# Kernel optimization log

Hardware: AMD Instinct MI355X
Metric: run time of the kernel (lower is better)

## Reference

```python
import jax, jax.numpy as jnp
import numpy as np

N = 50000      # nodes
E = 400000     # edges
IN = 128       # in_dim == emb_dim (residual requires equality)
POS = 64       # pos_in_dim
EMB = 128
LN_EPS = 1e-5


def _ln(x, g, b):
    m = jnp.mean(x, axis=-1, keepdims=True)
    v = jnp.mean((x - m) ** 2, axis=-1, keepdims=True)
    return (x - m) / jnp.sqrt(v + LN_EPS) * g + b


def _gin(x, src, dst, eps, W1, b1, g1, be1, W2, b2):
    # GINConv: mlp((1+eps)*x + sum_{j in N(i)} x_j)
    agg = jax.ops.segment_sum(x[src], dst, num_segments=x.shape[0])
    h = (1.0 + eps) * x + agg
    h = jax.nn.relu(_ln(h @ W1 + b1, g1, be1))
    return h @ W2 + b2


def setup_inputs() -> dict:
    key = jax.random.key(0)
    ks = jax.random.split(key, 8)
    x = jax.random.normal(ks[0], (N, IN), jnp.float32)
    pos = jax.random.normal(ks[1], (N, POS), jnp.float32)
    edge_index = jax.random.randint(ks[2], (2, E), 0, N)
    d = IN + POS
    f32 = jnp.float32
    W1 = (jax.random.normal(ks[3], (d, EMB), f32) / np.sqrt(d))
    W2 = (jax.random.normal(ks[4], (EMB, EMB), f32) / np.sqrt(EMB))
    W1p = (jax.random.normal(ks[5], (POS, EMB), f32) / np.sqrt(POS))
    W2p = (jax.random.normal(ks[6], (EMB, EMB), f32) / np.sqrt(EMB))
    z = jnp.zeros((EMB,), f32)
    o = jnp.ones((EMB,), f32)
    return {
        "x": x, "pos": pos, "edge_index": edge_index,
        "eps": jnp.zeros((), f32), "W1": W1, "b1": z, "g1": o, "be1": z,
        "W2": W2, "b2": z, "ln_g": o, "ln_b": z,
        "epsp": jnp.zeros((), f32), "W1p": W1p, "b1p": z, "g1p": o, "be1p": z,
        "W2p": W2p, "b2p": z, "lnp_g": o, "lnp_b": z,
    }


def reference(x, pos, edge_index, eps, W1, b1, g1, be1, W2, b2, ln_g, ln_b,
              epsp, W1p, b1p, g1p, be1p, W2p, b2p, lnp_g, lnp_b):
    src, dst = edge_index[0], edge_index[1]
    node_feats = jnp.concatenate([x, pos], axis=-1)  # [N, IN+POS]
    h = jax.nn.relu(_ln(_gin(node_feats, src, dst, eps, W1, b1, g1, be1, W2, b2), ln_g, ln_b))
    p = jax.nn.relu(_ln(_gin(pos, src, dst, epsp, W1p, b1p, g1p, be1p, W2p, b2p), lnp_g, lnp_b))
    # dropout is identity in eval mode (model_drop_ratio applied only when training)
    h = h + x  # add_residual=True
    return (h, p)
```

## Files before the change

### kernel.cpp

```cpp
#include <hip/hip_runtime.h>

#define NN    50000
#define NPAD  50048
#define HB    391
#define EE    400000
#define IND   128
#define POSD  64
#define DD    192
#define EMBD  128
#define LNEPS 1e-5f
#define CAP   32

#define FILLV_B 391
#define CAT_B   4692
#define WC_B    256

typedef __attribute__((ext_vector_type(8))) short bf16x8;
typedef __attribute__((ext_vector_type(4))) unsigned short u16x4;
typedef __attribute__((ext_vector_type(4))) float f32x4;
typedef unsigned short ushort_t;
typedef unsigned int uint_t;

#define MFMA16 __builtin_amdgcn_mfma_f32_16x16x32_bf16

__device__ inline ushort_t f2bf(float f) {
  union { float f; unsigned u; } v; v.f = f;
  unsigned r = (v.u + 0x7FFFu + ((v.u >> 16) & 1u)) >> 16;
  return (ushort_t)r;
}
__device__ inline float bf2f(unsigned u) {
  union { unsigned u; float f; } v; v.u = u << 16;
  return v.f;
}

__global__ __launch_bounds__(256) void prep_k(
    const float* __restrict__ x, const float* __restrict__ pos,
    const int* __restrict__ ei,
    const float* __restrict__ W1, const float* __restrict__ W2,
    const float* __restrict__ W1p, const float* __restrict__ W2p,
    int* __restrict__ cnt, int* __restrict__ csr,
    ushort_t* __restrict__ cat, ushort_t* __restrict__ wt) {
  const int bid = blockIdx.x;
  if (bid < FILLV_B) {
    int e0 = (bid * 256 + threadIdx.x) * 4;
    if (e0 >= EE) return;
    int4 s = *(const int4*)(ei + e0);
    int4 d = *(const int4*)(ei + EE + e0);
    int i0 = atomicAdd(&cnt[d.x], 1);
    int i1 = atomicAdd(&cnt[d.y], 1);
    int i2 = atomicAdd(&cnt[d.z], 1);
    int i3 = atomicAdd(&cnt[d.w], 1);
    if (i0 < CAP) csr[(size_t)d.x * CAP + i0] = s.x;
    if (i1 < CAP) csr[(size_t)d.y * CAP + i1] = s.y;
    if (i2 < CAP) csr[(size_t)d.z * CAP + i2] = s.z;
    if (i3 < CAP) csr[(size_t)d.w * CAP + i3] = s.w;
  } else if (bid < FILLV_B + CAT_B) {
    int id  = (bid - FILLV_B) * 256 + threadIdx.x;
    int n   = id / 24, sub = id - n * 24;
    bf16x8 o = (bf16x8){0, 0, 0, 0, 0, 0, 0, 0};
    if (n < NN) {
      const float* src = (sub < 16) ? (x + (size_t)n * IND + sub * 8)
                                    : (pos + (size_t)n * POSD + (sub - 16) * 8);
      f32x4 v0 = *(const f32x4*)(src);
      f32x4 v1 = *(const f32x4*)(src + 4);
#pragma unroll
      for (int i = 0; i < 4; ++i) {
        o[i]     = (short)f2bf(v0[i]);
        o[i + 4] = (short)f2bf(v1[i]);
      }
    }
    *(bf16x8*)(cat + (size_t)n * DD + sub * 8) = o;
  } else {
    int t = (bid - FILLV_B - CAT_B) * 256 + threadIdx.x;
    if (t < 24576) {
      int c = t / 192, k = t % 192;
      wt[t] = f2bf(W1[k * EMBD + c]);
    } else if (t < 40960) {
      int q = t - 24576; int c = q / 128, k = q % 128;
      wt[t] = f2bf(W2[k * EMBD + c]);
    } else if (t < 49152) {
      int q = t - 40960; int c = q / 64, k = q % 64;
      wt[t] = f2bf(W1p[k * EMBD + c]);
    } else {
      int q = t - 49152; int c = q / 128, k = q % 128;
      wt[t] = f2bf(W2p[k * EMBD + c]);
    }
  }
}

__global__ __launch_bounds__(256) void gather2_k(
    const ushort_t* __restrict__ cat, const int* __restrict__ cnt,
    const int* __restrict__ csr,
    const float* __restrict__ epsv, const float* __restrict__ epspv,
    ushort_t* __restrict__ h0, ushort_t* __restrict__ p0) {
  const int lane = threadIdx.x & 63;
  const int wv   = threadIdx.x >> 6;
  const int half = lane >> 5;
  const int l2   = lane & 31;
  const int n    = blockIdx.x * 8 + wv * 2 + half;

  int deg = 0;
  if (n < NN) { deg = cnt[n]; if (deg > CAP) deg = CAP; }
  int idx = (l2 < deg) ? csr[(size_t)n * CAP + l2] : NN;

  float a0 = 0.f, a1 = 0.f, a2 = 0.f, a3 = 0.f, a4 = 0.f, a5 = 0.f;
  for (int t = 0; t < deg; t += 8) {
    int s[8];
#pragma unroll
    for (int k = 0; k < 8; ++k) s[k] = __shfl(idx, half * 32 + t + k);
    u16x4 u[8]; uint_t v[8];
#pragma unroll
    for (int k = 0; k < 8; ++k) {
      int sk = (t + k < CAP) ? s[k] : NN;
      const ushort_t* r = cat + (size_t)sk * DD;
      u[k] = *(const u16x4*)(r + l2 * 4);
      v[k] = *(const uint_t*)(r + 128 + l2 * 2);
    }
#pragma unroll
    for (int k = 0; k < 8; ++k) {
      a0 += bf2f(u[k][0]); a1 += bf2f(u[k][1]);
      a2 += bf2f(u[k][2]); a3 += bf2f(u[k][3]);
      a4 += bf2f(v[k] & 0xffffu); a5 += bf2f(v[k] >> 16);
    }
  }

  const float e1  = 1.0f + epsv[0];
  const float ep1 = 1.0f + epspv[0];
  const ushort_t* self = cat + (size_t)n * DD;
  u16x4 su = *(const u16x4*)(self + l2 * 4);
  uint_t sv = *(const uint_t*)(self + 128 + l2 * 2);

  u16x4 o;
  o[0] = f2bf(fmaf(e1, bf2f(su[0]), a0));
  o[1] = f2bf(fmaf(e1, bf2f(su[1]), a1));
  o[2] = f2bf(fmaf(e1, bf2f(su[2]), a2));
  o[3] = f2bf(fmaf(e1, bf2f(su[3]), a3));
  *(u16x4*)(h0 + (size_t)n * DD + l2 * 4) = o;

  float p4 = bf2f(sv & 0xffffu), p5 = bf2f(sv >> 16);
  uint_t oh = (uint_t)f2bf(fmaf(e1, p4, a4)) |
              ((uint_t)f2bf(fmaf(e1, p5, a5)) << 16);
  *(uint_t*)(h0 + (size_t)n * DD + 128 + l2 * 2) = oh;
  uint_t op = (uint_t)f2bf(fmaf(ep1, p4, a4)) |
              ((uint_t)f2bf(fmaf(ep1, p5, a5)) << 16);
  *(uint_t*)(p0 + (size_t)n * POSD + l2 * 2) = op;
}

__device__ inline void ln_epi_T(f32x4 (&acc)[8][2],
                                const float* __restrict__ bias,
                                const float* __restrict__ gam,
                                const float* __restrict__ bet, int g) {
  f32x4 bv[8], gv[8], bev[8];
#pragma unroll
  for (int nt = 0; nt < 8; ++nt) {
    bv[nt]  = *(const f32x4*)(bias + nt * 16 + g * 4);
    gv[nt]  = *(const f32x4*)(gam  + nt * 16 + g * 4);
    bev[nt] = *(const f32x4*)(bet  + nt * 16 + g * 4);
  }
#pragma unroll
  for (int mt = 0; mt < 2; ++mt) {
    float s = 0.f, sq = 0.f;
#pragma unroll
    for (int nt = 0; nt < 8; ++nt)
#pragma unroll
      for (int r = 0; r < 4; ++r) {
        float v = acc[nt][mt][r] + bv[nt][r];
        acc[nt][mt][r] = v;
        s += v; sq += v * v;
      }
    s  += __shfl_xor(s, 16);  sq += __shfl_xor(sq, 16);
    s  += __shfl_xor(s, 32);  sq += __shfl_xor(sq, 32);
    float mean = s * (1.0f / 128.0f);
    float var  = sq * (1.0f / 128.0f) - mean * mean;
    float rstd = rsqrtf(var + LNEPS);
#pragma unroll
    for (int nt = 0; nt < 8; ++nt)
#pragma unroll
      for (int r = 0; r < 4; ++r)
        acc[nt][mt][r] = fmaxf(
            fmaf((acc[nt][mt][r] - mean) * rstd, gv[nt][r], bev[nt][r]), 0.f);
  }
}

__device__ inline void act_write_T(char* act, f32x4 (&acc)[8][2], int g, int c0) {
#pragma unroll
  for (int mt = 0; mt < 2; ++mt) {
    int lr = mt * 16 + c0;
    int sw = (lr & 7) << 4;
#pragma unroll
    for (int nt = 0; nt < 8; ++nt) {
      u16x4 o;
#pragma unroll
      for (int r = 0; r < 4; ++r) o[r] = f2bf(acc[nt][mt][r]);
      *(u16x4*)(act + lr * 256 + ((nt * 32 + g * 8) ^ sw)) = o;
    }
  }
}

#if __has_builtin(__builtin_amdgcn_global_load_lds)
__device__ inline void stage_w(const ushort_t* __restrict__ src, char* dst,
                               int rowbytes, int chunks, int tid, int wv) {
  int cpr = rowbytes >> 4;
  for (int k = 0; k < chunks; k += 256) {
    int c    = k + tid;
    int row  = c / cpr;
    int colb = ((c - row * cpr) << 4) ^ ((row & 7) << 4);
    const char* g = (const char*)src + row * rowbytes + colb;
    char* l = dst + (k + (wv << 6)) * 16;
    __builtin_amdgcn_global_load_lds(
        (const __attribute__((address_space(1))) void*)g,
        (__attribute__((address_space(3))) void*)l, 16, 0, 0);
  }
}
#else
__device__ inline void stage_w(const ushort_t* __restrict__ src, char* dst,
                               int rowbytes, int chunks, int tid, int wv) {
  int cpr = rowbytes >> 4;
  for (int i = tid; i < chunks; i += 256) {
    int row  = i / cpr;
    int colb = (i - row * cpr) << 4;
    *(bf16x8*)(dst + row * rowbytes + (colb ^ ((row & 7) << 4))) =
        *(const bf16x8*)(src + (size_t)i * 8);
  }
}
#endif

__global__ __launch_bounds__(256) void mlp_k(
    const ushort_t* __restrict__ h0, const ushort_t* __restrict__ p0,
    const ushort_t* __restrict__ wt,
    const float* __restrict__ b1, const float* __restrict__ g1,
    const float* __restrict__ be1,
    const float* __restrict__ b2, const float* __restrict__ lng,
    const float* __restrict__ lnb,
    const float* __restrict__ b1p, const float* __restrict__ g1p,
    const float* __restrict__ be1p,
    const float* __restrict__ b2p, const float* __restrict__ lnpg,
    const float* __restrict__ lnpb,
    const float* __restrict__ x, float* __restrict__ out) {
  __shared__ __align__(16) char smem[81920];
  const int tid  = threadIdx.x;
  const int lane = tid & 63;
  const int wv   = tid >> 6;
  const int g    = lane >> 4;
  const int c0   = lane & 15;
  const int bid  = blockIdx.x;

  f32x4 acc[8][2];

  if (bid < HB) {
    const int m0 = bid * 128;
    stage_w(wt, smem, 384, 3072, tid, wv);
    stage_w(wt + 24576, smem + 49152, 256, 2048, tid, wv);
    bf16x8 a0[6], a1[6];
    const size_t r0 = (size_t)(m0 + wv * 32 + c0) * DD;
    const size_t r1 = r0 + (size_t)16 * DD;
#pragma unroll
    for (int ks = 0; ks < 6; ++ks) {
      a0[ks] = *(const bf16x8*)(h0 + r0 + ks * 32 + g * 8);
      a1[ks] = *(const bf16x8*)(h0 + r1 + ks * 32 + g * 8);
    }
    __syncthreads();

#pragma unroll
    for (int nt = 0; nt < 8; ++nt)
#pragma unroll
      for (int mt = 0; mt < 2; ++mt) acc[nt][mt] = (f32x4){0.f, 0.f, 0.f, 0.f};
#pragma unroll
    for (int ks = 0; ks < 6; ++ks)
#pragma unroll
      for (int nt = 0; nt < 8; ++nt) {
        int wrow = nt * 16 + c0;
        bf16x8 w = *(const bf16x8*)(smem + wrow * 384 +
                                    ((ks * 64 + g * 16) ^ ((wrow & 7) << 4)));
        acc[nt][0] = MFMA16(w, a0[ks], acc[nt][0], 0, 0, 0);
        acc[nt][1] = MFMA16(w, a1[ks], acc[nt][1], 0, 0, 0);
      }
    ln_epi_T(acc, b1, g1, be1, g);
    __syncthreads();

    char* act = smem + wv * 8192;
    act_write_T(act, acc, g, c0);

#pragma unroll
    for (int nt = 0; nt < 8; ++nt)
#pragma unroll
      for (int mt = 0; mt < 2; ++mt) acc[nt][mt] = (f32x4){0.f, 0.f, 0.f, 0.f};
#pragma unroll
    for (int ks = 0; ks < 4; ++ks) {
      bf16x8 am[2];
#pragma unroll
      for (int mt = 0; mt < 2; ++mt) {
        int lr = mt * 16 + c0;
        am[mt] = *(const bf16x8*)(act + lr * 256 +
                                  ((ks * 64 + g * 16) ^ ((lr & 7) << 4)));
      }
#pragma unroll
      for (int nt = 0; nt < 8; ++nt) {
        int wrow = nt * 16 + c0;
        bf16x8 w = *(const bf16x8*)(smem + 49152 + wrow * 256 +
                                    ((ks * 64 + g * 16) ^ ((wrow & 7) << 4)));
        acc[nt][0] = MFMA16(w, am[0], acc[nt][0], 0, 0, 0);
        acc[nt][1] = MFMA16(w, am[1], acc[nt][1], 0, 0, 0);
      }
    }
    ln_epi_T(acc, b2, lng, lnb, g);
#pragma unroll
    for (int mt = 0; mt < 2; ++mt) {
      int node = m0 + wv * 32 + mt * 16 + c0;
      if (node < NN) {
#pragma unroll
        for (int nt = 0; nt < 8; ++nt) {
          int f0 = nt * 16 + g * 4;
          f32x4 xr = *(const f32x4*)(x + (size_t)node * IND + f0);
          f32x4 o;
#pragma unroll
          for (int r = 0; r < 4; ++r) o[r] = acc[nt][mt][r] + xr[r];
          *(f32x4*)(out + (size_t)node * EMBD + f0) = o;
        }
      }
    }
  } else {
    const int m0 = (bid - HB) * 128;
    stage_w(wt + 40960, smem, 128, 1024, tid, wv);
    stage_w(wt + 49152, smem + 16384, 256, 2048, tid, wv);
    bf16x8 a0[2], a1[2];
    const size_t r0 = (size_t)(m0 + wv * 32 + c0) * POSD;
    const size_t r1 = r0 + (size_t)16 * POSD;
#pragma unroll
    for (int ks = 0; ks < 2; ++ks) {
      a0[ks] = *(const bf16x8*)(p0 + r0 + ks * 32 + g * 8);
      a1[ks] = *(const bf16x8*)(p0 + r1 + ks * 32 + g * 8);
    }
    __syncthreads();

#pragma unroll
    for (int nt = 0; nt < 8; ++nt)
#pragma unroll
      for (int mt = 0; mt < 2; ++mt) acc[nt][mt] = (f32x4){0.f, 0.f, 0.f, 0.f};
#pragma unroll
    for (int ks = 0; ks < 2; ++ks)
#pragma unroll
      for (int nt = 0; nt < 8; ++nt) {
        int wrow = nt * 16 + c0;
        bf16x8 w = *(const bf16x8*)(smem + wrow * 128 +
                                    ((ks * 64 + g * 16) ^ ((wrow & 7) << 4)));
        acc[nt][0] = MFMA16(w, a0[ks], acc[nt][0], 0, 0, 0);
        acc[nt][1] = MFMA16(w, a1[ks], acc[nt][1], 0, 0, 0);
      }
    ln_epi_T(acc, b1p, g1p, be1p, g);

    char* act = smem + 49152 + wv * 8192;
    act_write_T(act, acc, g, c0);

#pragma unroll
    for (int nt = 0; nt < 8; ++nt)
#pragma unroll
      for (int mt = 0; mt < 2; ++mt) acc[nt][mt] = (f32x4){0.f, 0.f, 0.f, 0.f};
#pragma unroll
    for (int ks = 0; ks < 4; ++ks) {
      bf16x8 am[2];
#pragma unroll
      for (int mt = 0; mt < 2; ++mt) {
        int lr = mt * 16 + c0;
        am[mt] = *(const bf16x8*)(act + lr * 256 +
                                  ((ks * 64 + g * 16) ^ ((lr & 7) << 4)));
      }
#pragma unroll
      for (int nt = 0; nt < 8; ++nt) {
        int wrow = nt * 16 + c0;
        bf16x8 w = *(const bf16x8*)(smem + 16384 + wrow * 256 +
                                    ((ks * 64 + g * 16) ^ ((wrow & 7) << 4)));
        acc[nt][0] = MFMA16(w, am[0], acc[nt][0], 0, 0, 0);
        acc[nt][1] = MFMA16(w, am[1], acc[nt][1], 0, 0, 0);
      }
    }
    ln_epi_T(acc, b2p, lnpg, lnpb, g);
#pragma unroll
    for (int mt = 0; mt < 2; ++mt) {
      int node = m0 + wv * 32 + mt * 16 + c0;
      if (node < NN) {
#pragma unroll
        for (int nt = 0; nt < 8; ++nt) {
          int f0 = nt * 16 + g * 4;
          f32x4 o;
#pragma unroll
          for (int r = 0; r < 4; ++r) o[r] = acc[nt][mt][r];
          *(f32x4*)(out + (size_t)NN * EMBD + (size_t)node * EMBD + f0) = o;
        }
      }
    }
  }
}

extern "C" void kernel_launch(void* const* d_in, const int* in_sizes, int n_in,
                              void* d_out, int out_size, void* d_ws, size_t ws_size,
                              hipStream_t stream) {
  const float* x    = (const float*)d_in[0];
  const float* pos  = (const float*)d_in[1];
  const int*   ei   = (const int*)d_in[2];
  const float* eps  = (const float*)d_in[3];
  const float* W1   = (const float*)d_in[4];
  const float* b1   = (const float*)d_in[5];
  const float* g1   = (const float*)d_in[6];
  const float* be1  = (const float*)d_in[7];
  const float* W2   = (const float*)d_in[8];
  const float* b2   = (const float*)d_in[9];
  const float* lng  = (const float*)d_in[10];
  const float* lnb  = (const float*)d_in[11];
  const float* epsp = (const float*)d_in[12];
  const float* W1p  = (const float*)d_in[13];
  const float* b1p  = (const float*)d_in[14];
  const float* g1p  = (const float*)d_in[15];
  const float* be1p = (const float*)d_in[16];
  const float* W2p  = (const float*)d_in[17];
  const float* b2p  = (const float*)d_in[18];
  const float* lnpg = (const float*)d_in[19];
  const float* lnpb = (const float*)d_in[20];

  char* ws = (char*)d_ws;
  float* out = (float*)d_out;

  const size_t CATB = (size_t)NPAD * DD * 2;
  const size_t P0B  = (size_t)NPAD * POSD * 2;

  int*      cnt = (int*)ws;
  int*      csr = (int*)(ws + 200000);
  ushort_t* cat = (ushort_t*)(ws + 6600000);
  ushort_t* h0  = (ushort_t*)(ws + 6600000 + CATB);
  ushort_t* p0  = (ushort_t*)(ws + 6600000 + 2 * CATB);
  ushort_t* wt  = (ushort_t*)(ws + 6600000 + 2 * CATB + P0B);

  hipMemsetAsync(cnt, 0, (size_t)NN * sizeof(int), stream);
  prep_k<<<FILLV_B + CAT_B + WC_B, 256, 0, stream>>>(
      x, pos, ei, W1, W2, W1p, W2p, cnt, csr, cat, wt);
  gather2_k<<<NPAD / 8, 256, 0, stream>>>(cat, cnt, csr, eps, epsp, h0, p0);
  mlp_k<<<2 * HB, 256, 0, stream>>>(
      h0, p0, wt, b1, g1, be1, b2, lng, lnb,
      b1p, g1p, be1p, b2p, lnpg, lnpb, x, out);
}
```

Measured before the change: 105.1 us.

## Process two row tiles per MLP block and read W2 from global

The MLP kernel now assigns two 128-row tiles to each block, halving the grid so the W1 staging into LDS is amortised over twice the rows. The second tile's activations are prefetched into registers during the first tile's epilogue, and the residual x loads are issued before the final layernorm. W2 is no longer staged in LDS but read directly from global memory (relying on cache), and the activation scratch moves to a fixed LDS offset. The risks are fewer blocks (392) for the 256 CUs, higher register pressure from the prefetch buffers, and uncached-pattern global reads of W2 inside the MFMA loop.

```diff
diff --git a/kernel.cpp b/kernel.cpp
--- a/kernel.cpp
+++ b/kernel.cpp
@@ -3,6 +3,7 @@
 #define NN    50000
 #define NPAD  50048
 #define HB    391
+#define HB2   196
 #define EE    400000
 #define IND   128
 #define POSD  64
@@ -225,6 +226,70 @@
 }
 #endif
 
+__device__ inline void gemm1_192(const char* smem, const bf16x8 (&a0)[6],
+                                 const bf16x8 (&a1)[6], f32x4 (&acc)[8][2],
+                                 int g, int c0) {
+#pragma unroll
+  for (int nt = 0; nt < 8; ++nt)
+#pragma unroll
+    for (int mt = 0; mt < 2; ++mt) acc[nt][mt] = (f32x4){0.f, 0.f, 0.f, 0.f};
+#pragma unroll
+  for (int ks = 0; ks < 6; ++ks)
+#pragma unroll
+    for (int nt = 0; nt < 8; ++nt) {
+      int wrow = nt * 16 + c0;
+      bf16x8 w = *(const bf16x8*)(smem + wrow * 384 +
+                                  ((ks * 64 + g * 16) ^ ((wrow & 7) << 4)));
+      acc[nt][0] = MFMA16(w, a0[ks], acc[nt][0], 0, 0, 0);
+      acc[nt][1] = MFMA16(w, a1[ks], acc[nt][1], 0, 0, 0);
+    }
+}
+
+__device__ inline void gemm1_64(const char* smem, const bf16x8 (&a0)[2],
+                                const bf16x8 (&a1)[2], f32x4 (&acc)[8][2],
+                                int g, int c0) {
+#pragma unroll
+  for (int nt = 0; nt < 8; ++nt)
+#pragma unroll
+    for (int mt = 0; mt < 2; ++mt) acc[nt][mt] = (f32x4){0.f, 0.f, 0.f, 0.f};
+#pragma unroll
+  for (int ks = 0; ks < 2; ++ks)
+#pragma unroll
+    for (int nt = 0; nt < 8; ++nt) {
+      int wrow = nt * 16 + c0;
+      bf16x8 w = *(const bf16x8*)(smem + wrow * 128 +
+                                  ((ks * 64 + g * 16) ^ ((wrow & 7) << 4)));
+      acc[nt][0] = MFMA16(w, a0[ks], acc[nt][0], 0, 0, 0);
+      acc[nt][1] = MFMA16(w, a1[ks], acc[nt][1], 0, 0, 0);
+    }
+}
+
+__device__ inline void gemm2_g(const ushort_t* __restrict__ W2g,
+                               const char* act, f32x4 (&acc)[8][2],
+                               int g, int c0) {
+#pragma unroll
+  for (int nt = 0; nt < 8; ++nt)
+#pragma unroll
+    for (int mt = 0; mt < 2; ++mt) acc[nt][mt] = (f32x4){0.f, 0.f, 0.f, 0.f};
+#pragma unroll
+  for (int ks = 0; ks < 4; ++ks) {
+    bf16x8 am[2];
+#pragma unroll
+    for (int mt = 0; mt < 2; ++mt) {
+      int lr = mt * 16 + c0;
+      am[mt] = *(const bf16x8*)(act + lr * 256 +
+                                ((ks * 64 + g * 16) ^ ((lr & 7) << 4)));
+    }
+#pragma unroll
+    for (int nt = 0; nt < 8; ++nt) {
+      int wrow = nt * 16 + c0;
+      bf16x8 w = *(const bf16x8*)(W2g + (size_t)wrow * EMBD + ks * 32 + g * 8);
+      acc[nt][0] = MFMA16(w, am[0], acc[nt][0], 0, 0, 0);
+      acc[nt][1] = MFMA16(w, am[1], acc[nt][1], 0, 0, 0);
+    }
+  }
+}
+
 __global__ __launch_bounds__(256) void mlp_k(
     const ushort_t* __restrict__ h0, const ushort_t* __restrict__ p0,
     const ushort_t* __restrict__ wt,
@@ -244,148 +309,171 @@
   const int g    = lane >> 4;
   const int c0   = lane & 15;
   const int bid  = blockIdx.x;
+  char* act = smem + 49152 + wv * 8192;
 
   f32x4 acc[8][2];
 
-  if (bid < HB) {
-    const int m0 = bid * 128;
+  if (bid < HB2) {
+    const int t0 = bid * 2;
+    const bool t1ok = (t0 + 1) < HB;
+    const ushort_t* W2g = wt + 24576;
+
     stage_w(wt, smem, 384, 3072, tid, wv);
-    stage_w(wt + 24576, smem + 49152, 256, 2048, tid, wv);
     bf16x8 a0[6], a1[6];
-    const size_t r0 = (size_t)(m0 + wv * 32 + c0) * DD;
-    const size_t r1 = r0 + (size_t)16 * DD;
-#pragma unroll
-    for (int ks = 0; ks < 6; ++ks) {
-      a0[ks] = *(const bf16x8*)(h0 + r0 + ks * 32 + g * 8);
-      a1[ks] = *(const bf16x8*)(h0 + r1 + ks * 32 + g * 8);
+    {
+      const size_t r0 = (size_t)(t0 * 128 + wv * 32 + c0) * DD;
+#pragma unroll
+      for (int ks = 0; ks < 6; ++ks) {
+        a0[ks] = *(const bf16x8*)(h0 + r0 + ks * 32 + g * 8);
+        a1[ks] = *(const bf16x8*)(h0 + r0 + (size_t)16 * DD + ks * 32 + g * 8);
+      }
     }
     __syncthreads();
 
-#pragma unroll
-    for (int nt = 0; nt < 8; ++nt)
-#pragma unroll
-      for (int mt = 0; mt < 2; ++mt) acc[nt][mt] = (f32x4){0.f, 0.f, 0.f, 0.f};
-#pragma unroll
-    for (int ks = 0; ks < 6; ++ks)
-#pragma unroll
-      for (int nt = 0; nt < 8; ++nt) {
-        int wrow = nt * 16 + c0;
-        bf16x8 w = *(const bf16x8*)(smem + wrow * 384 +
-                                    ((ks * 64 + g * 16) ^ ((wrow & 7) << 4)));
-        acc[nt][0] = MFMA16(w, a0[ks], acc[nt][0], 0, 0, 0);
-        acc[nt][1] = MFMA16(w, a1[ks], acc[nt][1], 0, 0, 0);
-      }
+    gemm1_192(smem, a0, a1, acc, g, c0);
     ln_epi_T(acc, b1, g1, be1, g);
+
+    bf16x8 b0[6], b1f[6];
+    if (t1ok) {
+      const size_t r0 = (size_t)((t0 + 1) * 128 + wv * 32 + c0) * DD;
+#pragma unroll
+      for (int ks = 0; ks < 6; ++ks) {
+        b0[ks]  = *(const bf16x8*)(h0 + r0 + ks * 32 + g * 8);
+        b1f[ks] = *(const bf16x8*)(h0 + r0 + (size_t)16 * DD + ks * 32 + g * 8);
+      }
+    }
+
+    act_write_T(act, acc, g, c0);
+    gemm2_g(W2g, act, acc, g, c0);
+    {
+      const int m0 = t0 * 128;
+      f32x4 xr[2][8];
+#pragma unroll
+      for (int mt = 0; mt < 2; ++mt) {
+        int node = m0 + wv * 32 + mt * 16 + c0;
+        int nl   = node < NN ? node : NN - 1;
+#pragma unroll
+        for (int nt = 0; nt < 8; ++nt)
+          xr[mt][nt] = *(const f32x4*)(x + (size_t)nl * IND + nt * 16 + g * 4);
+      }
+      ln_epi_T(acc, b2, lng, lnb, g);
+#pragma unroll
+      for (int mt = 0; mt < 2; ++mt) {
+        int node = m0 + wv * 32 + mt * 16 + c0;
+        if (node < NN) {
+#pragma unroll
+          for (int nt = 0; nt < 8; ++nt) {
+            int f0 = nt * 16 + g * 4;
+            f32x4 o;
+#pragma unroll
+            for (int r = 0; r < 4; ++r) o[r] = acc[nt][mt][r] + xr[mt][nt][r];
+            *(f32x4*)(out + (size_t)node * EMBD + f0) = o;
+          }
+        }
+      }
+    }
+
+    if (t1ok) {
+      gemm1_192(smem, b0, b1f, acc, g, c0);
+      ln_epi_T(acc, b1, g1, be1, g);
+      act_write_T(act, acc, g, c0);
+      gemm2_g(W2g, act, acc, g, c0);
+      const int m0 = (t0 + 1) * 128;
+      f32x4 xr[2][8];
+#pragma unroll
+      for (int mt = 0; mt < 2; ++mt) {
+        int node = m0 + wv * 32 + mt * 16 + c0;
+        int nl   = node < NN ? node : NN - 1;
+#pragma unroll
+        for (int nt = 0; nt < 8; ++nt)
+          xr[mt][nt] = *(const f32x4*)(x + (size_t)nl * IND + nt * 16 + g * 4);
+      }
+      ln_epi_T(acc, b2, lng, lnb, g);
+#pragma unroll
+      for (int mt = 0; mt < 2; ++mt) {
+        int node = m0 + wv * 32 + mt * 16 + c0;
+        if (node < NN) {
+#pragma unroll
+          for (int nt = 0; nt < 8; ++nt) {
+            int f0 = nt * 16 + g * 4;
+            f32x4 o;
+#pragma unroll
+            for (int r = 0; r < 4; ++r) o[r] = acc[nt][mt][r] + xr[mt][nt][r];
+            *(f32x4*)(out + (size_t)node * EMBD + f0) = o;
+          }
+        }
+      }
+    }
+  } else {
+    const int t0 = (bid - HB2) * 2;
+    const bool t1ok = (t0 + 1) < HB;
+    const ushort_t* W2g = wt + 49152;
+
+    stage_w(wt + 40960, smem, 128, 1024, tid, wv);
+    bf16x8 a0[2], a1[2];
+    {
+      const size_t r0 = (size_t)(t0 * 128 + wv * 32 + c0) * POSD;
+#pragma unroll
+      for (int ks = 0; ks < 2; ++ks) {
+        a0[ks] = *(const bf16x8*)(p0 + r0 + ks * 32 + g * 8);
+        a1[ks] = *(const bf16x8*)(p0 + r0 + (size_t)16 * POSD + ks * 32 + g * 8);
+      }
+    }
     __syncthreads();
 
-    char* act = smem + wv * 8192;
+    gemm1_64(smem, a0, a1, acc, g, c0);
+    ln_epi_T(acc, b1p, g1p, be1p, g);
+
+    bf16x8 b0[2], b1f[2];
+    if (t1ok) {
+      const size_t r0 = (size_t)((t0 + 1) * 128 + wv * 32 + c0) * POSD;
+#pragma unroll
+      for (int ks = 0; ks < 2; ++ks) {
+        b0[ks]  = *(const bf16x8*)(p0 + r0 + ks * 32 + g * 8);
+        b1f[ks] = *(const bf16x8*)(p0 + r0 + (size_t)16 * POSD + ks * 32 + g * 8);
+      }
+    }
+
     act_write_T(act, acc, g, c0);
-
-#pragma unroll
-    for (int nt = 0; nt < 8; ++nt)
-#pragma unroll
-      for (int mt = 0; mt < 2; ++mt) acc[nt][mt] = (f32x4){0.f, 0.f, 0.f, 0.f};
-#pragma unroll
-    for (int ks = 0; ks < 4; ++ks) {
-      bf16x8 am[2];
+    gemm2_g(W2g, act, acc, g, c0);
+    ln_epi_T(acc, b2p, lnpg, lnpb, g);
+    {
+      const int m0 = t0 * 128;
 #pragma unroll
       for (int mt = 0; mt < 2; ++mt) {
-        int lr = mt * 16 + c0;
-        am[mt] = *(const bf16x8*)(act + lr * 256 +
-                                  ((ks * 64 + g * 16) ^ ((lr & 7) << 4)));
-      }
-#pragma unroll
-      for (int nt = 0; nt < 8; ++nt) {
-        int wrow = nt * 16 + c0;
-        bf16x8 w = *(const bf16x8*)(smem + 49152 + wrow * 256 +
-                                    ((ks * 64 + g * 16) ^ ((wrow & 7) << 4)));
-        acc[nt][0] = MFMA16(w, am[0], acc[nt][0], 0, 0, 0);
-        acc[nt][1] = MFMA16(w, am[1], acc[nt][1], 0, 0, 0);
-      }
-    }
-    ln_epi_T(acc, b2, lng, lnb, g);
-#pragma unroll
-    for (int mt = 0; mt < 2; ++mt) {
-      int node = m0 + wv * 32 + mt * 16 + c0;
-      if (node < NN) {
-#pragma unroll
-        for (int nt = 0; nt < 8; ++nt) {
-          int f0 = nt * 16 + g * 4;
-          f32x4 xr = *(const f32x4*)(x + (size_t)node * IND + f0);
-          f32x4 o;
-#pragma unroll
-          for (int r = 0; r < 4; ++r) o[r] = acc[nt][mt][r] + xr[r];
-          *(f32x4*)(out + (size_t)node * EMBD + f0) = o;
+        int node = m0 + wv * 32 + mt * 16 + c0;
+        if (node < NN) {
+#pragma unroll
+          for (int nt = 0; nt < 8; ++nt) {
+            int f0 = nt * 16 + g * 4;
+            f32x4 o;
+#pragma unroll
+            for (int r = 0; r < 4; ++r) o[r] = acc[nt][mt][r];
+            *(f32x4*)(out + (size_t)NN * EMBD + (size_t)node * EMBD + f0) = o;
+          }
         }
       }
     }
-  } else {
-    const int m0 = (bid - HB) * 128;
-    stage_w(wt + 40960, smem, 128, 1024, tid, wv);
-    stage_w(wt + 49152, smem + 16384, 256, 2048, tid, wv);
-    bf16x8 a0[2], a1[2];
-    const size_t r0 = (size_t)(m0 + wv * 32 + c0) * POSD;
-    const size_t r1 = r0 + (size_t)16 * POSD;
-#pragma unroll
-    for (int ks = 0; ks < 2; ++ks) {
-      a0[ks] = *(const bf16x8*)(p0 + r0 + ks * 32 + g * 8);
-      a1[ks] = *(const bf16x8*)(p0 + r1 + ks * 32 + g * 8);
-    }
-    __syncthreads();
-
-#pragma unroll
-    for (int nt = 0; nt < 8; ++nt)
-#pragma unroll
-      for (int mt = 0; mt < 2; ++mt) acc[nt][mt] = (f32x4){0.f, 0.f, 0.f, 0.f};
-#pragma unroll
-    for (int ks = 0; ks < 2; ++ks)
-#pragma unroll
-      for (int nt = 0; nt < 8; ++nt) {
-        int wrow = nt * 16 + c0;
-        bf16x8 w = *(const bf16x8*)(smem + wrow * 128 +
-                                    ((ks * 64 + g * 16) ^ ((wrow & 7) << 4)));
-        acc[nt][0] = MFMA16(w, a0[ks], acc[nt][0], 0, 0, 0);
-        acc[nt][1] = MFMA16(w, a1[ks], acc[nt][1], 0, 0, 0);
-      }
-    ln_epi_T(acc, b1p, g1p, be1p, g);
-
-    char* act = smem + 49152 + wv * 8192;
-    act_write_T(act, acc, g, c0);
-
-#pragma unroll
-    for (int nt = 0; nt < 8; ++nt)
-#pragma unroll
-      for (int mt = 0; mt < 2; ++mt) acc[nt][mt] = (f32x4){0.f, 0.f, 0.f, 0.f};
-#pragma unroll
-    for (int ks = 0; ks < 4; ++ks) {
-      bf16x8 am[2];
+
+    if (t1ok) {
+      gemm1_64(smem, b0, b1f, acc, g, c0);
+      ln_epi_T(acc, b1p, g1p, be1p, g);
+      act_write_T(act, acc, g, c0);
+      gemm2_g(W2g, act, acc, g, c0);
+      ln_epi_T(acc, b2p, lnpg, lnpb, g);
+      const int m0 = (t0 + 1) * 128;
 #pragma unroll
       for (int mt = 0; mt < 2; ++mt) {
-        int lr = mt * 16 + c0;
-        am[mt] = *(const bf16x8*)(act + lr * 256 +
-                                  ((ks * 64 + g * 16) ^ ((lr & 7) << 4)));
-      }
-#pragma unroll
-      for (int nt = 0; nt < 8; ++nt) {
-        int wrow = nt * 16 + c0;
-        bf16x8 w = *(const bf16x8*)(smem + 16384 + wrow * 256 +
-                                    ((ks * 64 + g * 16) ^ ((wrow & 7) << 4)));
-        acc[nt][0] = MFMA16(w, am[0], acc[nt][0], 0, 0, 0);
-        acc[nt][1] = MFMA16(w, am[1], acc[nt][1], 0, 0, 0);
-      }
-    }
-    ln_epi_T(acc, b2p, lnpg, lnpb, g);
-#pragma unroll
-    for (int mt = 0; mt < 2; ++mt) {
-      int node = m0 + wv * 32 + mt * 16 + c0;
-      if (node < NN) {
-#pragma unroll
-        for (int nt = 0; nt < 8; ++nt) {
-          int f0 = nt * 16 + g * 4;
-          f32x4 o;
-#pragma unroll
-          for (int r = 0; r < 4; ++r) o[r] = acc[nt][mt][r];
-          *(f32x4*)(out + (size_t)NN * EMBD + (size_t)node * EMBD + f0) = o;
+        int node = m0 + wv * 32 + mt * 16 + c0;
+        if (node < NN) {
+#pragma unroll
+          for (int nt = 0; nt < 8; ++nt) {
+            int f0 = nt * 16 + g * 4;
+            f32x4 o;
+#pragma unroll
+            for (int r = 0; r < 4; ++r) o[r] = acc[nt][mt][r];
+            *(f32x4*)(out + (size_t)NN * EMBD + (size_t)node * EMBD + f0) = o;
+          }
         }
       }
     }
@@ -434,7 +522,7 @@
   prep_k<<<FILLV_B + CAT_B + WC_B, 256, 0, stream>>>(
       x, pos, ei, W1, W2, W1p, W2p, cnt, csr, cat, wt);
   gather2_k<<<NPAD / 8, 256, 0, stream>>>(cat, cnt, csr, eps, epsp, h0, p0);
-  mlp_k<<<2 * HB, 256, 0, stream>>>(
+  mlp_k<<<2 * HB2, 256, 0, stream>>>(
       h0, p0, wt, b1, g1, be1, b2, lng, lnb,
       b1p, g1p, be1p, b2p, lnpg, lnpb, x, out);
 }
```

Result: slower. 112.0 us (+6.6%).
